# Kernel tuning notes

Hardware: AMD Instinct MI355X
Metric: run time of the kernel (lower is better)

## Reference

```python
import jax, jax.numpy as jnp
import numpy as np

N_NODES = 65536
N_EDGES = 1048576
D = 128           # input_dim == hidden_dim*heads, residual active everywhere
HEADS = (4, 4, 1) # heads per GATv2 layer; last layer heads=1, out=input_dim
NUM_LAYERS = 3


def setup_inputs() -> dict:
    key = jax.random.key(0)
    ks = jax.random.split(key, 16)
    x = jax.random.normal(ks[0], (N_NODES, D), dtype=jnp.float32)
    edge_src = jax.random.randint(ks[1], (N_EDGES,), 0, N_NODES)
    edge_dst = jax.random.randint(ks[2], (N_EDGES,), 0, N_NODES)
    edge_attr = jax.random.uniform(ks[3], (N_EDGES, 1), dtype=jnp.float32)
    s = 0.05
    Wl = jax.random.normal(ks[4], (NUM_LAYERS, D, D), dtype=jnp.float32) * s
    bl = jnp.zeros((NUM_LAYERS, D), dtype=jnp.float32)
    Wr = jax.random.normal(ks[5], (NUM_LAYERS, D, D), dtype=jnp.float32) * s
    br = jnp.zeros((NUM_LAYERS, D), dtype=jnp.float32)
    We = jax.random.normal(ks[6], (NUM_LAYERS, 1, D), dtype=jnp.float32) * s
    att = jax.random.normal(ks[7], (NUM_LAYERS, D), dtype=jnp.float32) * s  # reshaped (H,C) per layer
    bias_p = jnp.zeros((NUM_LAYERS, D), dtype=jnp.float32)
    ln_g = jnp.ones((NUM_LAYERS, D), dtype=jnp.float32)
    ln_b = jnp.zeros((NUM_LAYERS, D), dtype=jnp.float32)
    return {"x": x, "edge_src": edge_src, "edge_dst": edge_dst, "edge_attr": edge_attr,
            "Wl": Wl, "bl": bl, "Wr": Wr, "br": br, "We": We, "att": att,
            "bias_p": bias_p, "ln_g": ln_g, "ln_b": ln_b, "num_graphs": 128}


def _layer_norm(x, g, b):
    mu = x.mean(-1, keepdims=True)
    var = jnp.mean((x - mu) ** 2, axis=-1, keepdims=True)
    return (x - mu) * jax.lax.rsqrt(var + 1e-5) * g + b


def _gatv2(x, src, dst, ea, Wl, bl, Wr, br, We, att, bias, H):
    # GATv2Conv, eval mode (no dropout), concat heads
    N = x.shape[0]
    HC = Wl.shape[1]
    C = HC // H
    xl = (x @ Wl + bl).reshape(N, H, C)
    xr = (x @ Wr + br).reshape(N, H, C)
    ee = (ea @ We).reshape(-1, H, C)            # [E, H, C]
    m = xl[src] + xr[dst] + ee                  # gather + fuse edge features
    m = jnp.where(m >= 0, m, 0.2 * m)           # leaky_relu(0.2)
    a = jnp.einsum('ehc,hc->eh', m, att.reshape(H, C))
    # scatter-softmax over destination node neighborhoods
    amax = jax.ops.segment_max(a, dst, num_segments=N)
    ae = jnp.exp(a - amax[dst])
    asum = jax.ops.segment_sum(ae, dst, num_segments=N)
    alpha = ae / (asum[dst] + 1e-16)
    out = jax.ops.segment_sum(xl[src] * alpha[:, :, None], dst, num_segments=N)
    return out.reshape(N, HC) + bias


def reference(x, edge_src, edge_dst, edge_attr, Wl, bl, Wr, br, We, att,
              bias_p, ln_g, ln_b, num_graphs):
    N = x.shape[0]
    # add_self_loops=True with fill_value='mean' for edge_attr (PyG default)
    loop = jnp.arange(N, dtype=edge_src.dtype)
    src = jnp.concatenate([edge_src, loop])
    dst = jnp.concatenate([edge_dst, loop])
    ea_mean = edge_attr.mean(0, keepdims=True)
    ea = jnp.concatenate([edge_attr, jnp.broadcast_to(ea_mean, (N, edge_attr.shape[1]))])
    h = x
    for i in range(NUM_LAYERS):
        out = _gatv2(h, src, dst, ea, Wl[i], bl[i], Wr[i], br[i], We[i],
                     att[i], bias_p[i], HEADS[i])
        out = _layer_norm(out, ln_g[i], ln_b[i])
        if i < NUM_LAYERS - 1:
            out = jax.nn.gelu(out, approximate=False)
        h = h + out  # residual: dims match at every layer by construction
    # to_dense_batch with equal-size graphs, then drop virtual node (last per graph)
    x_dense = h.reshape(num_graphs, -1, h.shape[-1])
    return x_dense[:, :-1, :]
```

## Files before the change

kernel.cpp:

```cpp
#include <hip/hip_runtime.h>
#include <hip/hip_bf16.h>

typedef unsigned int uint;
typedef unsigned short ushort;

#define NN 65536
#define NE 1048576
#define DD 128
#define TOTE (NE + NN)

__device__ __forceinline__ float b2f(ushort u) {
    uint v = ((uint)u) << 16; float f; __builtin_memcpy(&f, &v, 4); return f;
}
__device__ __forceinline__ ushort f2b(float f) {
    uint x; __builtin_memcpy(&x, &f, 4);
    uint r = (x + 0x7fffu + ((x >> 16) & 1u)) >> 16;
    return (ushort)r;
}

typedef __bf16 bf16x8 __attribute__((ext_vector_type(8)));
typedef float f32x4 __attribute__((ext_vector_type(4)));
typedef float f32x2 __attribute__((ext_vector_type(2)));

__device__ __forceinline__ f32x2 bf2f2(uint u) {
    union { uint i; float f; } lo, hi;
    lo.i = u << 16; hi.i = u & 0xffff0000u;
    return (f32x2){lo.f, hi.f};
}


__global__ void k_init(const float* __restrict__ Wl, const float* __restrict__ Wr,
                       ushort* __restrict__ WT, int* __restrict__ cnt, float* __restrict__ sumbuf,
                       float* __restrict__ cano) {
    if (cano && blockIdx.x == 0 && blockIdx.y == 0 && blockIdx.z == 0 && threadIdx.x == 0)
        cano[0] = 100.0f;
    int k = blockIdx.x, n = threadIdx.x, lr = blockIdx.y, layer = blockIdx.z;
    const float* W = (lr ? Wr : Wl) + layer * 16384;
    WT[(layer * 2 + lr) * 16384 + n * 128 + k] = f2b(W[k * 128 + n]);
    int gid = ((blockIdx.z * 2 + blockIdx.y) * 128 + blockIdx.x) * 128 + threadIdx.x;
    if (gid < NN) cnt[gid] = 0;
    if (gid == NN) sumbuf[0] = 0.f;
}

__global__ void k_histsum(const int* __restrict__ dst, const float* __restrict__ ea,
                          int* __restrict__ cnt, float* __restrict__ sum,
                          float* __restrict__ cano) {
    if (cano && blockIdx.x == 0 && threadIdx.x == 0) cano[1] = 120.0f;
    __shared__ float red[256];
    int t = threadIdx.x;
    int e = blockIdx.x * 256 + t;
    int d = (e < NE) ? dst[e] : (e - NE);
    atomicAdd(&cnt[d], 1);
    float s = (e < NE) ? ea[e] : 0.f;
    red[t] = s; __syncthreads();
    for (int o = 128; o > 0; o >>= 1) { if (t < o) red[t] += red[t + o]; __syncthreads(); }
    if (t == 0 && red[0] != 0.f) atomicAdd(sum, red[0]);
}

__global__ void k_scanA(const int* __restrict__ cnt, int* __restrict__ row_off, int* __restrict__ bsum,
                        float* __restrict__ cano) {
    if (cano && blockIdx.x == 0 && threadIdx.x == 0) cano[2] = 140.0f;
    __shared__ int tmp[256];
    int t = threadIdx.x, i = blockIdx.x * 256 + t;
    int v = cnt[i]; tmp[t] = v; __syncthreads();
    for (int off = 1; off < 256; off <<= 1) {
        int x = (t >= off) ? tmp[t - off] : 0;
        __syncthreads();
        tmp[t] += x;
        __syncthreads();
    }
    row_off[i] = tmp[t] - v;
    if (t == 255) bsum[blockIdx.x] = tmp[255];
}

__global__ void k_scanC(int* __restrict__ row_off, const int* __restrict__ bsum, int* __restrict__ cursor,
                        float* __restrict__ cano) {
    if (cano && blockIdx.x == 0 && threadIdx.x == 0) cano[3] = 160.0f;
    __shared__ int tmp[256];
    __shared__ int excl[256];
    int t = threadIdx.x;
    int v = bsum[t]; tmp[t] = v; __syncthreads();
    for (int off = 1; off < 256; off <<= 1) {
        int x = (t >= off) ? tmp[t - off] : 0;
        __syncthreads();
        tmp[t] += x;
        __syncthreads();
    }
    excl[t] = tmp[t] - v;
    __syncthreads();
    int offb = excl[blockIdx.x];
    int i = blockIdx.x * 256 + t;
    int nv = row_off[i] + offb;
    row_off[i] = nv;
    cursor[i] = nv;
    if (i == 0) row_off[NN] = TOTE;
}

__global__ void k_scatter(const int* __restrict__ src, const int* __restrict__ dst,
                          const float* __restrict__ ea, const float* __restrict__ sum,
                          int* __restrict__ cursor, int2* __restrict__ adj,
                          float* __restrict__ cano) {
    if (cano && blockIdx.x == 0 && threadIdx.x == 0) cano[4] = 180.0f;
    int e = blockIdx.x * 256 + threadIdx.x;
    int s, d; float a;
    if (e < NE) { s = src[e]; d = dst[e]; a = ea[e]; }
    else        { s = e - NE; d = s;      a = sum[0] * (1.0f / NE); }
    int pos = atomicAdd(&cursor[d], 1);
    adj[pos] = make_int2(s << 8, __float_as_int(a));
}

template<bool F32SRC>
__global__ __launch_bounds__(512) void k_gemm(const void* __restrict__ srcv, const ushort* __restrict__ WT,
                                              const float* __restrict__ bl, const float* __restrict__ br,
                                              ushort* __restrict__ xl, ushort* __restrict__ xr,
                                              float* __restrict__ cano, int cslot, float cval) {
    if (cano && blockIdx.x == 0 && threadIdx.x == 0) cano[cslot] = cval;
    __shared__ __align__(16) ushort S[32768];

    int t = threadIdx.x;
    int rowbase = blockIdx.x * 128;

    #pragma unroll
    for (int i = 0; i < 8; i++) {
        int idx = i * 512 + t;
        int m = idx >> 11, n = (idx >> 4) & 127, c = idx & 15;
        *(bf16x8*)&S[m * 16384 + c * 1024 + n * 8] =
            *(const bf16x8*)&WT[m * 16384 + n * 128 + c * 8];
    }

    int wave = t >> 6, lane = t & 63;
    int row16 = lane & 15, quad = lane >> 4;
    int myrow = rowbase + wave * 16 + row16;

    float bbl[8], bbr[8];
    #pragma unroll
    for (int tc = 0; tc < 8; tc++) { bbl[tc] = bl[tc * 16 + row16]; bbr[tc] = br[tc * 16 + row16]; }

    f32x4 accl[8], accr[8];
    #pragma unroll
    for (int i = 0; i < 8; i++) {
        accl[i] = (f32x4){0.f, 0.f, 0.f, 0.f};
        accr[i] = (f32x4){0.f, 0.f, 0.f, 0.f};
    }

    __syncthreads();

    #pragma unroll
    for (int ks = 0; ks < 4; ks++) {
        bf16x8 a;
        if (F32SRC) {
            const float* src = (const float*)srcv;
            const float* pa = &src[(size_t)myrow * 128 + ks * 32 + quad * 8];
            float4 v0 = *(const float4*)pa;
            float4 v1 = *(const float4*)(pa + 4);
            ushort u[8] = {f2b(v0.x), f2b(v0.y), f2b(v0.z), f2b(v0.w),
                           f2b(v1.x), f2b(v1.y), f2b(v1.z), f2b(v1.w)};
            __builtin_memcpy(&a, u, 16);
        } else {
            a = *(const bf16x8*)&((const ushort*)srcv)[(size_t)myrow * 128 + ks * 32 + quad * 8];
        }
        int chunk = ks * 4 + quad;
        #pragma unroll
        for (int tc = 0; tc < 8; tc++) {
            int coln = tc * 16 + row16;
            bf16x8 b_l = *(const bf16x8*)&S[chunk * 1024 + coln * 8];
            bf16x8 b_r = *(const bf16x8*)&S[16384 + chunk * 1024 + coln * 8];
            accl[tc] = __builtin_amdgcn_mfma_f32_16x16x32_bf16(a, b_l, accl[tc], 0, 0, 0);
            accr[tc] = __builtin_amdgcn_mfma_f32_16x16x32_bf16(a, b_r, accr[tc], 0, 0, 0);
        }
    }

    __syncthreads();

    #pragma unroll
    for (int tc = 0; tc < 8; tc++) {
        int col = tc * 16 + row16;
        #pragma unroll
        for (int r = 0; r < 4; r++) {
            int row = wave * 16 + quad * 4 + r;
            S[row * 128 + col]         = f2b(accl[tc][r] + bbl[tc]);
            S[16384 + row * 128 + col] = f2b(accr[tc][r] + bbr[tc]);
        }
    }
    __syncthreads();

    #pragma unroll
    for (int i = 0; i < 8; i++) {
        int idx = i * 512 + t;
        int m = idx >> 11, row = (idx >> 4) & 127, c8 = idx & 15;
        bf16x8 v = *(const bf16x8*)&S[m * 16384 + row * 128 + c8 * 8];
        ushort* dst = m ? xr : xl;
        *(bf16x8*)&dst[(size_t)(rowbase + row) * 128 + c8 * 8] = v;
    }
}

template<int H, bool FINAL>
__global__ __launch_bounds__(128, 4) void k_attn(
    const ushort* __restrict__ xl, const ushort* __restrict__ xr,
    const int* __restrict__ row_off, const int2* __restrict__ adj,
    const float* __restrict__ We, const float* __restrict__ att,
    const float* __restrict__ bias, const float* __restrict__ ln_g, const float* __restrict__ ln_b,
    const float* __restrict__ hin, float* __restrict__ hout, ushort* __restrict__ hb,
    float* __restrict__ outp,
    float* __restrict__ cano, int cslot, float cval)
{
    if (cano && blockIdx.x == 0 && threadIdx.x == 0) cano[cslot] = cval;
    __shared__ float accbuf[2][8][160];

    int wv = threadIdx.x >> 6, lane = threadIdx.x & 63;
    int n = blockIdx.x * 2 + wv;
    int p = lane >> 3;
    int cl = lane & 7;
    int c16 = cl * 16;
    const char* xlb = (const char*)xl;

    f32x2 we2[8], at2[8], xrl2[8];
    #pragma unroll
    for (int k = 0; k < 8; k++) {
        we2[k] = (f32x2){We[c16 + 2 * k], We[c16 + 2 * k + 1]};
        at2[k] = (f32x2){att[c16 + 2 * k], att[c16 + 2 * k + 1]};
    }
    {
        uint4 r0 = *(const uint4*)&xr[(size_t)n * 128 + c16];
        uint4 r1 = *(const uint4*)&xr[(size_t)n * 128 + c16 + 8];
        xrl2[0] = bf2f2(r0.x); xrl2[1] = bf2f2(r0.y); xrl2[2] = bf2f2(r0.z); xrl2[3] = bf2f2(r0.w);
        xrl2[4] = bf2f2(r1.x); xrl2[5] = bf2f2(r1.y); xrl2[6] = bf2f2(r1.z); xrl2[7] = bf2f2(r1.w);
    }

    int s0 = row_off[n], s1 = row_off[n + 1];
    int iters = (s1 - s0 + 7) >> 3;

    float l_run = 0.f;
    f32x2 acc[8];
    #pragma unroll
    for (int k = 0; k < 8; k++) acc[k] = (f32x2){0.f, 0.f};

    int j0 = s0 + p,      j1 = s0 + 8 + p,  j2 = s0 + 16 + p, j3 = s0 + 24 + p;
    int i0 = (j0 < s1) ? j0 : s0;
    int i1 = (j1 < s1) ? j1 : s0;
    int i2 = (j2 < s1) ? j2 : s0;
    int i3 = (j3 < s1) ? j3 : s0;
    int2 a0 = adj[i0], a1 = adj[i1], a2 = adj[i2], a3 = adj[i3];
    float ea0 = (j0 < s1) ? __int_as_float(a0.y) : 0.f;
    float ea1 = (j1 < s1) ? __int_as_float(a1.y) : 0.f;
    float ea2v = (j2 < s1) ? __int_as_float(a2.y) : 0.f;
    float ea3 = (j3 < s1) ? __int_as_float(a3.y) : 0.f;
    const char* q0 = xlb + (size_t)(uint)a0.x + (cl << 5);
    const char* q1 = xlb + (size_t)(uint)a1.x + (cl << 5);
    const char* q2 = xlb + (size_t)(uint)a2.x + (cl << 5);
    const char* q3 = xlb + (size_t)(uint)a3.x + (cl << 5);
    uint4 u00 = *(const uint4*)q0, u01 = *(const uint4*)(q0 + 16);
    uint4 u10 = *(const uint4*)q1, u11 = *(const uint4*)(q1 + 16);
    uint4 u20 = *(const uint4*)q2, u21 = *(const uint4*)(q2 + 16);
    uint4 u30 = *(const uint4*)q3, u31 = *(const uint4*)(q3 + 16);

    auto consume = [&](uint4 u0, uint4 u1, float ea_c, int itx) {
        bool valid = (s0 + itx * 8 + p) < s1;
        f32x2 xf[8];
        xf[0] = bf2f2(u0.x); xf[1] = bf2f2(u0.y); xf[2] = bf2f2(u0.z); xf[3] = bf2f2(u0.w);
        xf[4] = bf2f2(u1.x); xf[5] = bf2f2(u1.y); xf[6] = bf2f2(u1.z); xf[7] = bf2f2(u1.w);

        f32x2 ea2 = (f32x2){ea_c, ea_c};
        f32x2 s2 = (f32x2){0.f, 0.f};
        #pragma unroll
        for (int k = 0; k < 8; k++) {
            f32x2 m = xf[k] + __builtin_elementwise_fma(ea2, we2[k], xrl2[k]);
            m = __builtin_elementwise_max(m, 0.2f * m);
            s2 = __builtin_elementwise_fma(m, at2[k], s2);
        }
        float s = s2.x + s2.y;
        s += __shfl_xor(s, 1);
        if (H == 1) { s += __shfl_xor(s, 2); s += __shfl_xor(s, 4); }
        if (!valid) s = -1e30f;

        float e = __expf(s);
        l_run += e;
        f32x2 e2 = (f32x2){e, e};
        #pragma unroll
        for (int k = 0; k < 8; k++) acc[k] = __builtin_elementwise_fma(e2, xf[k], acc[k]);
    };

    consume(u00, u01, ea0, 0);
    if (iters > 1) consume(u10, u11, ea1, 1);
    if (iters > 2) consume(u20, u21, ea2v, 2);
    if (iters > 3) consume(u30, u31, ea3, 3);
    for (int it = 4; it < iters; ++it) {
        int jn = s0 + it * 8 + p;
        int jb = (jn < s1) ? jn : s0;
        int2 pk = adj[jb];
        float ean = (jn < s1) ? __int_as_float(pk.y) : 0.f;
        const char* rp = xlb + (size_t)(uint)pk.x + (cl << 5);
        uint4 nu0 = *(const uint4*)rp;
        uint4 nu1 = *(const uint4*)(rp + 16);
        consume(nu0, nu1, ean, it);
    }

    l_run += __shfl_xor(l_run, 8);
    l_run += __shfl_xor(l_run, 16);
    l_run += __shfl_xor(l_run, 32);
    float inv = 1.0f / (l_run + 1e-16f);

    float* row = &accbuf[wv][p][cl * 20];
    #pragma unroll
    for (int i = 0; i < 4; i++)
        *(float4*)&row[4 * i] = make_float4(acc[2 * i].x * inv, acc[2 * i].y * inv,
                                            acc[2 * i + 1].x * inv, acc[2 * i + 1].y * inv);
    __syncthreads();

    int c0 = 2 * lane;
    int rb = (c0 >> 4) * 20 + (c0 & 15);
    float o0 = 0.f, o1 = 0.f;
    #pragma unroll
    for (int q = 0; q < 8; q++) {
        float2 v = *(float2*)&accbuf[wv][q][rb];
        o0 += v.x; o1 += v.y;
    }
    o0 += bias[c0];
    o1 += bias[c0 + 1];

    float sred = o0 + o1;
    #pragma unroll
    for (int off = 1; off < 64; off <<= 1) sred += __shfl_xor(sred, off);
    float mu = sred * (1.f / 128.f);
    float d0 = o0 - mu, d1 = o1 - mu;
    float v = d0 * d0 + d1 * d1;
    #pragma unroll
    for (int off = 1; off < 64; off <<= 1) v += __shfl_xor(v, off);
    float rstd = rsqrtf(v * (1.f / 128.f) + 1e-5f);
    o0 = d0 * rstd * ln_g[c0] + ln_b[c0];
    o1 = d1 * rstd * ln_g[c0 + 1] + ln_b[c0 + 1];

    float2 hv = *(const float2*)&hin[(size_t)n * 128 + c0];
    if (FINAL) {
        float r0 = hv.x + o0, r1 = hv.y + o1;
        int g = n >> 9, rr = n & 511;
        if (rr < 511)
            *(float2*)&outp[((size_t)(g * 511 + rr)) * 128 + c0] = make_float2(r0, r1);
    } else {
        o0 = 0.5f * o0 * (1.f + erff(o0 * 0.70710678118f));
        o1 = 0.5f * o1 * (1.f + erff(o1 * 0.70710678118f));
        hv.x += o0; hv.y += o1;
        *(float2*)&hout[(size_t)n * 128 + c0] = hv;
        uint pk = (uint)f2b(hv.x) | ((uint)f2b(hv.y) << 16);
        *(uint*)&hb[(size_t)n * 128 + c0] = pk;
    }
}

extern "C" void kernel_launch(void* const* d_in, const int* in_sizes, int n_in,
                              void* d_out, int out_size, void* d_ws, size_t ws_size,
                              hipStream_t stream) {
    const float* x        = (const float*)d_in[0];
    const int*   edge_src = (const int*)d_in[1];
    const int*   edge_dst = (const int*)d_in[2];
    const float* edge_attr= (const float*)d_in[3];
    const float* Wl       = (const float*)d_in[4];
    const float* bl       = (const float*)d_in[5];
    const float* Wr       = (const float*)d_in[6];
    const float* br       = (const float*)d_in[7];
    const float* We       = (const float*)d_in[8];
    const float* att      = (const float*)d_in[9];
    const float* bias_p   = (const float*)d_in[10];
    const float* ln_g     = (const float*)d_in[11];
    const float* ln_b     = (const float*)d_in[12];
    float* out = (float*)d_out;

    char* ws = (char*)d_ws;
    float*  h       = (float*)(ws + 0);
    ushort* hb      = (ushort*)(ws + 33554432);
    ushort* xl      = (ushort*)(ws + 50331648);
    ushort* xr      = (ushort*)(ws + 67108864);
    int2*   adj     = (int2*)(ws + 83886080);
    int*    row_off = (int*)(ws + 92798976);
    int*    cnt     = (int*)(ws + 93061376);
    int*    bsum    = (int*)(ws + 93323520);
    float*  sumbuf  = (float*)(ws + 93324544);
    ushort* WT      = (ushort*)(ws + 93324800);

    k_init<<<dim3(128, 2, 3), 128, 0, stream>>>(Wl, Wr, WT, cnt, sumbuf, out);
    k_histsum<<<TOTE / 256, 256, 0, stream>>>(edge_dst, edge_attr, cnt, sumbuf, out);
    k_scanA<<<NN / 256, 256, 0, stream>>>(cnt, row_off, bsum, out);
    k_scanC<<<NN / 256, 256, 0, stream>>>(row_off, bsum, cnt, out);
    k_scatter<<<TOTE / 256, 256, 0, stream>>>(edge_src, edge_dst, edge_attr, sumbuf, cnt, adj, out);

    k_gemm<true><<<NN / 128, 512, 0, stream>>>(x, WT, bl, br, xl, xr, out, 5, 200.0f);
    k_attn<4, false><<<NN / 2, 128, 0, stream>>>(xl, xr, row_off, adj,
                                                 We, att, bias_p, ln_g, ln_b,
                                                 x, h, hb, nullptr, out, 6, 220.0f);
    k_gemm<false><<<NN / 128, 512, 0, stream>>>(hb, WT + 32768, bl + 128, br + 128, xl, xr, out, 7, 240.0f);
    k_attn<4, false><<<NN / 2, 128, 0, stream>>>(xl, xr, row_off, adj,
                                                 We + 128, att + 128, bias_p + 128,
                                                 ln_g + 128, ln_b + 128,
                                                 h, h, hb, nullptr, out, 8, 260.0f);
    k_gemm<false><<<NN / 128, 512, 0, stream>>>(hb, WT + 65536, bl + 256, br + 256, xl, xr, out, 9, 280.0f);
    k_attn<1, true><<<NN / 2, 128, 0, stream>>>(xl, xr, row_off, adj,
                                                We + 256, att + 256, bias_p + 256,
                                                ln_g + 256, ln_b + 256,
                                                h, nullptr, nullptr, out, nullptr, 0, 0.0f);
}
```

Measured before the change: 537.6 us.

## Vectorize edge preprocessing, prefetch GEMM A operands, use tanh-approx GELU

The histogram and scatter kernels now handle four edges per thread with int4/float4 loads, and their grids shrink to match. The GEMM loads all of a thread's A-operand rows into registers before the MFMA loop, so global latency is exposed once instead of per k-step. The exact erf GELU is replaced by a tanh approximation written as x*sigmoid, using fast exp and fast divide. The GELU swap alters numerics slightly, and the prefetch raises register pressure.

```diff
diff --git a/kernel.cpp b/kernel.cpp
--- a/kernel.cpp
+++ b/kernel.cpp
@@ -48,10 +48,19 @@
     if (cano && blockIdx.x == 0 && threadIdx.x == 0) cano[1] = 120.0f;
     __shared__ float red[256];
     int t = threadIdx.x;
-    int e = blockIdx.x * 256 + t;
-    int d = (e < NE) ? dst[e] : (e - NE);
-    atomicAdd(&cnt[d], 1);
-    float s = (e < NE) ? ea[e] : 0.f;
+    int e0 = (blockIdx.x * 256 + t) * 4;
+    float s = 0.f;
+    if (e0 < NE) {
+        int4  d4 = *(const int4*)&dst[e0];
+        float4 a4 = *(const float4*)&ea[e0];
+        atomicAdd(&cnt[d4.x], 1); atomicAdd(&cnt[d4.y], 1);
+        atomicAdd(&cnt[d4.z], 1); atomicAdd(&cnt[d4.w], 1);
+        s = (a4.x + a4.y) + (a4.z + a4.w);
+    } else {
+        int b = e0 - NE;
+        atomicAdd(&cnt[b], 1);     atomicAdd(&cnt[b + 1], 1);
+        atomicAdd(&cnt[b + 2], 1); atomicAdd(&cnt[b + 3], 1);
+    }
     red[t] = s; __syncthreads();
     for (int o = 128; o > 0; o >>= 1) { if (t < o) red[t] += red[t + o]; __syncthreads(); }
     if (t == 0 && red[0] != 0.f) atomicAdd(sum, red[0]);
@@ -101,12 +110,24 @@
                           int* __restrict__ cursor, int2* __restrict__ adj,
                           float* __restrict__ cano) {
     if (cano && blockIdx.x == 0 && threadIdx.x == 0) cano[4] = 180.0f;
-    int e = blockIdx.x * 256 + threadIdx.x;
-    int s, d; float a;
-    if (e < NE) { s = src[e]; d = dst[e]; a = ea[e]; }
-    else        { s = e - NE; d = s;      a = sum[0] * (1.0f / NE); }
-    int pos = atomicAdd(&cursor[d], 1);
-    adj[pos] = make_int2(s << 8, __float_as_int(a));
+    int e0 = (blockIdx.x * 256 + threadIdx.x) * 4;
+    if (e0 < NE) {
+        int4  s4 = *(const int4*)&src[e0];
+        int4  d4 = *(const int4*)&dst[e0];
+        float4 a4 = *(const float4*)&ea[e0];
+        int p0 = atomicAdd(&cursor[d4.x], 1); adj[p0] = make_int2(s4.x << 8, __float_as_int(a4.x));
+        int p1 = atomicAdd(&cursor[d4.y], 1); adj[p1] = make_int2(s4.y << 8, __float_as_int(a4.y));
+        int p2 = atomicAdd(&cursor[d4.z], 1); adj[p2] = make_int2(s4.z << 8, __float_as_int(a4.z));
+        int p3 = atomicAdd(&cursor[d4.w], 1); adj[p3] = make_int2(s4.w << 8, __float_as_int(a4.w));
+    } else {
+        int b = e0 - NE;
+        float a = sum[0] * (1.0f / NE);
+        #pragma unroll
+        for (int k = 0; k < 4; k++) {
+            int p = atomicAdd(&cursor[b + k], 1);
+            adj[p] = make_int2((b + k) << 8, __float_as_int(a));
+        }
+    }
 }
 
 template<bool F32SRC>
@@ -132,6 +153,29 @@
     int row16 = lane & 15, quad = lane >> 4;
     int myrow = rowbase + wave * 16 + row16;
 
+    bf16x8 areg[4];
+    if (F32SRC) {
+        const float* src = (const float*)srcv;
+        float4 av[8];
+        #pragma unroll
+        for (int ks = 0; ks < 4; ks++) {
+            const float* pa = &src[(size_t)myrow * 128 + ks * 32 + quad * 8];
+            av[2 * ks]     = *(const float4*)pa;
+            av[2 * ks + 1] = *(const float4*)(pa + 4);
+        }
+        #pragma unroll
+        for (int ks = 0; ks < 4; ks++) {
+            ushort u[8] = {f2b(av[2 * ks].x), f2b(av[2 * ks].y), f2b(av[2 * ks].z), f2b(av[2 * ks].w),
+                           f2b(av[2 * ks + 1].x), f2b(av[2 * ks + 1].y), f2b(av[2 * ks + 1].z), f2b(av[2 * ks + 1].w)};
+            __builtin_memcpy(&areg[ks], u, 16);
+        }
+    } else {
+        const ushort* src = (const ushort*)srcv;
+        #pragma unroll
+        for (int ks = 0; ks < 4; ks++)
+            areg[ks] = *(const bf16x8*)&src[(size_t)myrow * 128 + ks * 32 + quad * 8];
+    }
+
     float bbl[8], bbr[8];
     #pragma unroll
     for (int tc = 0; tc < 8; tc++) { bbl[tc] = bl[tc * 16 + row16]; bbr[tc] = br[tc * 16 + row16]; }
@@ -147,26 +191,14 @@
 
     #pragma unroll
     for (int ks = 0; ks < 4; ks++) {
-        bf16x8 a;
-        if (F32SRC) {
-            const float* src = (const float*)srcv;
-            const float* pa = &src[(size_t)myrow * 128 + ks * 32 + quad * 8];
-            float4 v0 = *(const float4*)pa;
-            float4 v1 = *(const float4*)(pa + 4);
-            ushort u[8] = {f2b(v0.x), f2b(v0.y), f2b(v0.z), f2b(v0.w),
-                           f2b(v1.x), f2b(v1.y), f2b(v1.z), f2b(v1.w)};
-            __builtin_memcpy(&a, u, 16);
-        } else {
-            a = *(const bf16x8*)&((const ushort*)srcv)[(size_t)myrow * 128 + ks * 32 + quad * 8];
-        }
         int chunk = ks * 4 + quad;
         #pragma unroll
         for (int tc = 0; tc < 8; tc++) {
             int coln = tc * 16 + row16;
             bf16x8 b_l = *(const bf16x8*)&S[chunk * 1024 + coln * 8];
             bf16x8 b_r = *(const bf16x8*)&S[16384 + chunk * 1024 + coln * 8];
-            accl[tc] = __builtin_amdgcn_mfma_f32_16x16x32_bf16(a, b_l, accl[tc], 0, 0, 0);
-            accr[tc] = __builtin_amdgcn_mfma_f32_16x16x32_bf16(a, b_r, accr[tc], 0, 0, 0);
+            accl[tc] = __builtin_amdgcn_mfma_f32_16x16x32_bf16(areg[ks], b_l, accl[tc], 0, 0, 0);
+            accr[tc] = __builtin_amdgcn_mfma_f32_16x16x32_bf16(areg[ks], b_r, accr[tc], 0, 0, 0);
         }
     }
 
@@ -337,8 +369,10 @@
         if (rr < 511)
             *(float2*)&outp[((size_t)(g * 511 + rr)) * 128 + c0] = make_float2(r0, r1);
     } else {
-        o0 = 0.5f * o0 * (1.f + erff(o0 * 0.70710678118f));
-        o1 = 0.5f * o1 * (1.f + erff(o1 * 0.70710678118f));
+        float t0 = o0 * (0.79788456f + 0.03567741f * o0 * o0);
+        o0 = __fdividef(o0, 1.f + __expf(-2.f * t0));
+        float t1 = o1 * (0.79788456f + 0.03567741f * o1 * o1);
+        o1 = __fdividef(o1, 1.f + __expf(-2.f * t1));
         hv.x += o0; hv.y += o1;
         *(float2*)&hout[(size_t)n * 128 + c0] = hv;
         uint pk = (uint)f2b(hv.x) | ((uint)f2b(hv.y) << 16);
@@ -377,10 +411,10 @@
     ushort* WT      = (ushort*)(ws + 93324800);
 
     k_init<<<dim3(128, 2, 3), 128, 0, stream>>>(Wl, Wr, WT, cnt, sumbuf, out);
-    k_histsum<<<TOTE / 256, 256, 0, stream>>>(edge_dst, edge_attr, cnt, sumbuf, out);
+    k_histsum<<<TOTE / 1024, 256, 0, stream>>>(edge_dst, edge_attr, cnt, sumbuf, out);
     k_scanA<<<NN / 256, 256, 0, stream>>>(cnt, row_off, bsum, out);
     k_scanC<<<NN / 256, 256, 0, stream>>>(row_off, bsum, cnt, out);
-    k_scatter<<<TOTE / 256, 256, 0, stream>>>(edge_src, edge_dst, edge_attr, sumbuf, cnt, adj, out);
+    k_scatter<<<TOTE / 1024, 256, 0, stream>>>(edge_src, edge_dst, edge_attr, sumbuf, cnt, adj, out);
 
     k_gemm<true><<<NN / 128, 512, 0, stream>>>(x, WT, bl, br, xl, xr, out, 5, 200.0f);
     k_attn<4, false><<<NN / 2, 128, 0, stream>>>(xl, xr, row_off, adj,
```

After: 520.9 us. -3.1%, faster.
